# Kernel optimization log

Hardware: AMD Instinct MI355X
Metric: run time of the kernel (lower is better)

Reference implementation:

```python
import jax, jax.numpy as jnp
import numpy as np

B, N, D, H, O, K, N_USER, C = 1, 4096, 64, 4, 64, 2, 4000, 2


def setup_inputs() -> dict:
    key = jax.random.key(0)
    ks = jax.random.split(key, 7)
    h = jax.random.normal(ks[0], (B, N, D), jnp.float32)
    # dense 0/1 adjacency per heterogeneous kind, with self-loops so no row is empty
    adj = jax.random.randint(ks[1], (K, B, N, N), 0, 2).astype(jnp.float32)
    hadj = jnp.maximum(adj, jnp.eye(N, dtype=jnp.float32))
    s = 1.0 / np.sqrt(D).astype(np.float32)
    w = jax.random.normal(ks[2], (K, H, D, O), jnp.float32) * s
    a_src = jax.random.normal(ks[3], (K, H, O, 1), jnp.float32) * (1.0 / np.sqrt(O).astype(np.float32))
    a_dst = jax.random.normal(ks[4], (K, H, O, 1), jnp.float32) * (1.0 / np.sqrt(O).astype(np.float32))
    fc_w = jax.random.normal(ks[5], (C, O * K), jnp.float32) * (1.0 / np.sqrt(O * K).astype(np.float32))
    fc_b = jnp.zeros((C,), jnp.float32)
    return {"h": h, "hadj": hadj, "w": w, "a_src": a_src, "a_dst": a_dst, "fc_w": fc_w, "fc_b": fc_b}


def _gat(h, adj, w_k, a_src_k, a_dst_k):
    # h: (B,N,D); adj: (B,N,N); w_k: (H,D,O); a_*: (H,O,1)
    h_prime = jnp.einsum('bnf,hfo->bhno', h, w_k)          # (B,H,N,O)
    t = jnp.tanh(h_prime)
    attn_src = jnp.einsum('bhno,hoi->bhni', t, a_src_k)    # (B,H,N,1)
    attn_dst = jnp.einsum('bhno,hoi->bhni', t, a_dst_k)    # (B,H,N,1)
    attn = attn_src + jnp.swapaxes(attn_dst, -1, -2)       # (B,H,N,N) broadcast add
    attn = jnp.where(attn >= 0, attn, 0.2 * attn)          # LeakyReLU(0.2)
    attn = jnp.where(adj[:, None] > 0, attn, -jnp.inf)     # dense mask
    attn = jax.nn.softmax(attn, axis=-1)                   # dropout is a no-op in eval
    out = jnp.einsum('bhnm,bhmo->bhno', attn, h_prime)     # (B,H,N,O)
    return out.mean(axis=1)                                # mean over heads -> (B,N,O)


def reference(h, hadj, w, a_src, a_dst, fc_w, fc_b):
    embs = []
    for k in range(K):  # small fixed loop over heterogeneous node kinds
        x = _gat(h, hadj[k], w[k], a_src[k], a_dst[k])
        embs.append(x[:, :N_USER])
    type_aware = jnp.concatenate(embs, axis=-1)            # (B, N_USER, K*O)
    logits = type_aware @ fc_w.T + fc_b                    # (B, N_USER, C)
    return jax.nn.log_softmax(logits, axis=-1)
```

## Files before the change

### kernel.cpp

```cpp
#include <hip/hip_runtime.h>
#include <math.h>

constexpr int KK = 2;
constexpr int HH = 4;
constexpr int NN = 4096;
constexpr int DD = 64;
constexpr int OO = 64;
constexpr int NU = 4000;
constexpr int CC = 2;
constexpr int JSPLIT = 8;
constexpr int JCHUNK = NN / JSPLIT;
constexpr int NTILE = JCHUNK / 16;
constexpr float LOG2E = 1.44269504088896340736f;

typedef float vf4 __attribute__((ext_vector_type(4)));

__device__ __forceinline__ float fexp2(float x) {
#if __has_builtin(__builtin_amdgcn_exp2f)
  return __builtin_amdgcn_exp2f(x);
#else
  return exp2f(x);
#endif
}
__device__ __forceinline__ float frcp(float x) {
#if __has_builtin(__builtin_amdgcn_rcpf)
  return __builtin_amdgcn_rcpf(x);
#else
  return 1.0f / x;
#endif
}
__device__ __forceinline__ float ftanh(float x) {
  float e = fexp2(x * (2.0f * LOG2E));
  return 1.0f - 2.0f * frcp(e + 1.0f);
}

__global__ __launch_bounds__(256) void gat_phase1(
    const float* __restrict__ hsrc, const float* __restrict__ w,
    const float* __restrict__ a_src, const float* __restrict__ a_dst,
    const float* __restrict__ fc_w,
    float* __restrict__ src_s, float* __restrict__ att_d,
    float* __restrict__ att_g0, float* __restrict__ att_g1) {
  const int kh = blockIdx.y;
  const int k = kh >> 2;
  const int i0 = blockIdx.x * 64;
  const int tid = threadIdx.x;

  __shared__ float h_s[DD][68];
  __shared__ float w_s[DD][OO];

  {
    const float4* wp = (const float4*)(w + (size_t)kh * DD * OO);
    float4* ws4 = (float4*)w_s;
    for (int t = tid; t < DD * OO / 4; t += 256) ws4[t] = wp[t];
  }
  for (int t = tid; t < 1024; t += 256) {
    const int row = t >> 4;
    const int f4 = (t & 15) * 4;
    float4 v = *(const float4*)(hsrc + (size_t)(i0 + row) * DD + f4);
    h_s[f4 + 0][row] = v.x;
    h_s[f4 + 1][row] = v.y;
    h_s[f4 + 2][row] = v.z;
    h_s[f4 + 3][row] = v.w;
  }
  __syncthreads();

  const int og = tid & 15;
  const int rg = tid >> 4;
  const int o0 = og * 4;
  const int r0 = rg * 4;

  float hp[4][4];
#pragma unroll
  for (int j = 0; j < 4; ++j)
#pragma unroll
    for (int u = 0; u < 4; ++u) hp[j][u] = 0.0f;

#pragma unroll 8
  for (int f = 0; f < DD; ++f) {
    float4 hv = *(const float4*)&h_s[f][r0];
    float4 wv = *(const float4*)&w_s[f][o0];
    hp[0][0] = fmaf(hv.x, wv.x, hp[0][0]);
    hp[0][1] = fmaf(hv.x, wv.y, hp[0][1]);
    hp[0][2] = fmaf(hv.x, wv.z, hp[0][2]);
    hp[0][3] = fmaf(hv.x, wv.w, hp[0][3]);
    hp[1][0] = fmaf(hv.y, wv.x, hp[1][0]);
    hp[1][1] = fmaf(hv.y, wv.y, hp[1][1]);
    hp[1][2] = fmaf(hv.y, wv.z, hp[1][2]);
    hp[1][3] = fmaf(hv.y, wv.w, hp[1][3]);
    hp[2][0] = fmaf(hv.z, wv.x, hp[2][0]);
    hp[2][1] = fmaf(hv.z, wv.y, hp[2][1]);
    hp[2][2] = fmaf(hv.z, wv.z, hp[2][2]);
    hp[2][3] = fmaf(hv.z, wv.w, hp[2][3]);
    hp[3][0] = fmaf(hv.w, wv.x, hp[3][0]);
    hp[3][1] = fmaf(hv.w, wv.y, hp[3][1]);
    hp[3][2] = fmaf(hv.w, wv.z, hp[3][2]);
    hp[3][3] = fmaf(hv.w, wv.w, hp[3][3]);
  }

  float as[4], ad[4], f0[4], f1[4];
#pragma unroll
  for (int u = 0; u < 4; ++u) {
    as[u] = a_src[kh * OO + o0 + u];
    ad[u] = a_dst[kh * OO + o0 + u];
    f0[u] = fc_w[0 * (KK * OO) + k * OO + o0 + u];
    f1[u] = fc_w[1 * (KK * OO) + k * OO + o0 + u];
  }

#pragma unroll
  for (int j = 0; j < 4; ++j) {
    float sp = 0.0f, dp = 0.0f, g0 = 0.0f, g1 = 0.0f;
#pragma unroll
    for (int u = 0; u < 4; ++u) {
      float v = hp[j][u];
      float t = ftanh(v);
      sp = fmaf(t, as[u], sp);
      dp = fmaf(t, ad[u], dp);
      g0 = fmaf(v, f0[u], g0);
      g1 = fmaf(v, f1[u], g1);
    }
#pragma unroll
    for (int off = 1; off < 16; off <<= 1) {
      sp += __shfl_xor(sp, off, 64);
      dp += __shfl_xor(dp, off, 64);
      g0 += __shfl_xor(g0, off, 64);
      g1 += __shfl_xor(g1, off, 64);
    }
    if (og == 0) {
      const int i = i0 + r0 + j;
      src_s[kh * NN + i] = sp * LOG2E;
      att_d[kh * NN + i] = dp * LOG2E;
      att_g0[kh * NN + i] = g0;
      att_g1[kh * NN + i] = g1;
    }
  }
}

__global__ __launch_bounds__(256) void gat_phase2(
    const float* __restrict__ adj, const float* __restrict__ src_s,
    const float* __restrict__ att_d, const float* __restrict__ att_g0,
    const float* __restrict__ att_g1, float* __restrict__ P) {
  const int k = blockIdx.y >> 3;
  const int chunk = blockIdx.y & 7;
  const int r0 = blockIdx.x * 16;
  const int tid = threadIdx.x;
  const int wave = tid >> 6;
  const int lane = tid & 63;
  const int row = lane & 15;
  const int jsub = lane >> 4;
  const int i = r0 + row;
  const int j0 = chunk * JCHUNK;

  __shared__ float lds_att[12][JCHUNK];
  {
    const float* planes[3] = {att_d, att_g0, att_g1};
#pragma unroll
    for (int step = 0; step < 6; ++step) {
      const int fi = step * 256 + tid;
      const int v = fi >> 7;
      const int pos = (fi & 127) * 4;
      const int p = v >> 2, h = v & 3;
      vf4 val = *(const vf4*)(planes[p] + (size_t)(k * HH + h) * NN + j0 + pos);
      *(vf4*)&lds_att[v][pos] = val;
    }
  }

  float sreg[4];
#pragma unroll
  for (int h = 0; h < 4; ++h) sreg[h] = src_s[(k * HH + h) * NN + i];

  float l[4], a0[4], a1[4];
#pragma unroll
  for (int h = 0; h < 4; ++h) {
    l[h] = 0.0f;
    a0[h] = 0.0f;
    a1[h] = 0.0f;
  }

  __syncthreads();

  const float* arow = adj + (size_t)k * NN * NN + (size_t)i * NN + j0 + jsub * 4;
  vf4 apre0 = *(const vf4*)(arow + (wave + 0) * 16);
  vf4 apre1 = *(const vf4*)(arow + (wave + 4) * 16);

#pragma unroll
  for (int s = 0; s < 8; ++s) {
    const int t = wave + s * 4;
    const vf4 av = apre0;
    apre0 = apre1;
    if (s < 6) apre1 = *(const vf4*)(arow + (t + 8) * 16);
    const int jloc = jsub * 4 + t * 16;
#pragma unroll
    for (int h = 0; h < 4; ++h) {
      vf4 dv = *(const vf4*)&lds_att[0 * 4 + h][jloc];
      vf4 g0v = *(const vf4*)&lds_att[1 * 4 + h][jloc];
      vf4 g1v = *(const vf4*)&lds_att[2 * 4 + h][jloc];
#pragma unroll
      for (int jj = 0; jj < 4; ++jj) {
        float s2 = sreg[h] + dv[jj];
        float sl = fmaxf(s2, 0.2f * s2);
        float p = av[jj] * fexp2(sl);
        l[h] += p;
        a0[h] = fmaf(p, g0v[jj], a0[h]);
        a1[h] = fmaf(p, g1v[jj], a1[h]);
      }
    }
  }

#pragma unroll
  for (int h = 0; h < 4; ++h) {
    l[h] += __shfl_xor(l[h], 16, 64);
    l[h] += __shfl_xor(l[h], 32, 64);
    a0[h] += __shfl_xor(a0[h], 16, 64);
    a0[h] += __shfl_xor(a0[h], 32, 64);
    a1[h] += __shfl_xor(a1[h], 16, 64);
    a1[h] += __shfl_xor(a1[h], 32, 64);
  }

  __shared__ float sred[4][12][16];
  if (lane < 16) {
#pragma unroll
    for (int h = 0; h < 4; ++h) {
      sred[wave][h * 3 + 0][row] = l[h];
      sred[wave][h * 3 + 1][row] = a0[h];
      sred[wave][h * 3 + 2][row] = a1[h];
    }
  }
  __syncthreads();
  if (tid < 192) {
    const int v = tid >> 4;
    const int rr = tid & 15;
    float sum =
        sred[0][v][rr] + sred[1][v][rr] + sred[2][v][rr] + sred[3][v][rr];
    const int h = v / 3, c = v % 3;
    size_t base =
        ((((size_t)(k * JSPLIT + chunk) * HH + h) * 3 + c)) * NU + (r0 + rr);
    P[base] = sum;
  }
}

__global__ __launch_bounds__(256) void gat_phase3(
    const float* __restrict__ P, const float* __restrict__ fc_b,
    float* __restrict__ out) {
  const int i = blockIdx.x * 256 + threadIdx.x;
  if (i >= NU) return;
  float l0 = fc_b[0], l1 = fc_b[1];
#pragma unroll
  for (int k = 0; k < KK; ++k) {
#pragma unroll
    for (int q = 0; q < HH; ++q) {
      float ls = 0.0f, a0 = 0.0f, a1 = 0.0f;
#pragma unroll
      for (int ch = 0; ch < JSPLIT; ++ch) {
        size_t b = (((size_t)(k * JSPLIT + ch) * HH + q) * 3) * NU + i;
        ls += P[b];
        a0 += P[b + NU];
        a1 += P[b + 2 * (size_t)NU];
      }
      float inv = 1.0f / ls;
      l0 = fmaf(0.25f * a0, inv, l0);
      l1 = fmaf(0.25f * a1, inv, l1);
    }
  }
  float m = fmaxf(l0, l1);
  float lse = m + logf(expf(l0 - m) + expf(l1 - m));
  out[i * CC + 0] = l0 - lse;
  out[i * CC + 1] = l1 - lse;
}

extern "C" void kernel_launch(void* const* d_in, const int* in_sizes, int n_in,
                              void* d_out, int out_size, void* d_ws, size_t ws_size,
                              hipStream_t stream) {
  const float* hsrc  = (const float*)d_in[0];
  const float* hadj  = (const float*)d_in[1];
  const float* w     = (const float*)d_in[2];
  const float* a_src = (const float*)d_in[3];
  const float* a_dst = (const float*)d_in[4];
  const float* fc_w  = (const float*)d_in[5];
  const float* fc_b  = (const float*)d_in[6];
  float* out = (float*)d_out;

  char* ws = (char*)d_ws;
  float* src_s  = (float*)(ws + 0 * 131072);
  float* att_d  = (float*)(ws + 1 * 131072);
  float* att_g0 = (float*)(ws + 2 * 131072);
  float* att_g1 = (float*)(ws + 3 * 131072);
  float* P      = (float*)(ws + 4 * 131072);

  dim3 g1(NN / 64, KK * HH);
  gat_phase1<<<g1, 256, 0, stream>>>(hsrc, w, a_src, a_dst, fc_w,
                                     src_s, att_d, att_g0, att_g1);
  dim3 g2(NU / 16, KK * JSPLIT);
  gat_phase2<<<g2, 256, 0, stream>>>(hadj, src_s, att_d, att_g0, att_g1, P);
  gat_phase3<<<(NU + 255) / 256, 256, 0, stream>>>(P, fc_b, out);
}
```

Measured before the change: 222.7 us.

## Retile phase2 to 32 rows per block with packed float2 math

Phase 2 now handles 32 rows per block instead of 16. Each lane walks a row with 8-wide j stripes, so the per-row shuffle reduction drops to a single xor step and each LDS tile of attention coefficients is reused across twice as many rows. The LeakyReLU is rewritten as 0.6x + 0.4|x| and the accumulators use float2 vectors so the compiler can emit packed FMA instructions. Phase 1 is retiled to 32 rows per block for more blocks. The cost is that adjacency loads per lane are now 32-byte strided segments, which may hurt global coalescing, and phase 2 launches half as many blocks.

```diff
diff --git a/kernel.cpp b/kernel.cpp
--- a/kernel.cpp
+++ b/kernel.cpp
@@ -10,10 +10,10 @@
 constexpr int CC = 2;
 constexpr int JSPLIT = 8;
 constexpr int JCHUNK = NN / JSPLIT;
-constexpr int NTILE = JCHUNK / 16;
 constexpr float LOG2E = 1.44269504088896340736f;
 
 typedef float vf4 __attribute__((ext_vector_type(4)));
+typedef float vf2 __attribute__((ext_vector_type(2)));
 
 __device__ __forceinline__ float fexp2(float x) {
 #if __has_builtin(__builtin_amdgcn_exp2f)
@@ -42,21 +42,23 @@
     float* __restrict__ att_g0, float* __restrict__ att_g1) {
   const int kh = blockIdx.y;
   const int k = kh >> 2;
-  const int i0 = blockIdx.x * 64;
+  const int i0 = blockIdx.x * 32;
   const int tid = threadIdx.x;
 
-  __shared__ float h_s[DD][68];
+  __shared__ float h_s[DD][36];
   __shared__ float w_s[DD][OO];
 
   {
-    const float4* wp = (const float4*)(w + (size_t)kh * DD * OO);
-    float4* ws4 = (float4*)w_s;
+    const vf4* wp = (const vf4*)(w + (size_t)kh * DD * OO);
+    vf4* ws4 = (vf4*)w_s;
+#pragma unroll
     for (int t = tid; t < DD * OO / 4; t += 256) ws4[t] = wp[t];
   }
-  for (int t = tid; t < 1024; t += 256) {
+#pragma unroll
+  for (int t = tid; t < 512; t += 256) {
     const int row = t >> 4;
     const int f4 = (t & 15) * 4;
-    float4 v = *(const float4*)(hsrc + (size_t)(i0 + row) * DD + f4);
+    vf4 v = *(const vf4*)(hsrc + (size_t)(i0 + row) * DD + f4);
     h_s[f4 + 0][row] = v.x;
     h_s[f4 + 1][row] = v.y;
     h_s[f4 + 2][row] = v.z;
@@ -67,18 +69,18 @@
   const int og = tid & 15;
   const int rg = tid >> 4;
   const int o0 = og * 4;
-  const int r0 = rg * 4;
-
-  float hp[4][4];
-#pragma unroll
-  for (int j = 0; j < 4; ++j)
+  const int r0 = rg * 2;
+
+  float hp[2][4];
+#pragma unroll
+  for (int j = 0; j < 2; ++j)
 #pragma unroll
     for (int u = 0; u < 4; ++u) hp[j][u] = 0.0f;
 
 #pragma unroll 8
   for (int f = 0; f < DD; ++f) {
-    float4 hv = *(const float4*)&h_s[f][r0];
-    float4 wv = *(const float4*)&w_s[f][o0];
+    vf2 hv = *(const vf2*)&h_s[f][r0];
+    vf4 wv = *(const vf4*)&w_s[f][o0];
     hp[0][0] = fmaf(hv.x, wv.x, hp[0][0]);
     hp[0][1] = fmaf(hv.x, wv.y, hp[0][1]);
     hp[0][2] = fmaf(hv.x, wv.z, hp[0][2]);
@@ -87,14 +89,6 @@
     hp[1][1] = fmaf(hv.y, wv.y, hp[1][1]);
     hp[1][2] = fmaf(hv.y, wv.z, hp[1][2]);
     hp[1][3] = fmaf(hv.y, wv.w, hp[1][3]);
-    hp[2][0] = fmaf(hv.z, wv.x, hp[2][0]);
-    hp[2][1] = fmaf(hv.z, wv.y, hp[2][1]);
-    hp[2][2] = fmaf(hv.z, wv.z, hp[2][2]);
-    hp[2][3] = fmaf(hv.z, wv.w, hp[2][3]);
-    hp[3][0] = fmaf(hv.w, wv.x, hp[3][0]);
-    hp[3][1] = fmaf(hv.w, wv.y, hp[3][1]);
-    hp[3][2] = fmaf(hv.w, wv.z, hp[3][2]);
-    hp[3][3] = fmaf(hv.w, wv.w, hp[3][3]);
   }
 
   float as[4], ad[4], f0[4], f1[4];
@@ -107,7 +101,7 @@
   }
 
 #pragma unroll
-  for (int j = 0; j < 4; ++j) {
+  for (int j = 0; j < 2; ++j) {
     float sp = 0.0f, dp = 0.0f, g0 = 0.0f, g1 = 0.0f;
 #pragma unroll
     for (int u = 0; u < 4; ++u) {
@@ -141,12 +135,12 @@
     const float* __restrict__ att_g1, float* __restrict__ P) {
   const int k = blockIdx.y >> 3;
   const int chunk = blockIdx.y & 7;
-  const int r0 = blockIdx.x * 16;
+  const int r0 = blockIdx.x * 32;
   const int tid = threadIdx.x;
   const int wave = tid >> 6;
   const int lane = tid & 63;
-  const int row = lane & 15;
-  const int jsub = lane >> 4;
+  const int row = lane & 31;
+  const int jsub = lane >> 5;
   const int i = r0 + row;
   const int j0 = chunk * JCHUNK;
 
@@ -164,60 +158,77 @@
     }
   }
 
-  float sreg[4];
-#pragma unroll
-  for (int h = 0; h < 4; ++h) sreg[h] = src_s[(k * HH + h) * NN + i];
-
-  float l[4], a0[4], a1[4];
+  vf2 sreg2[4];
 #pragma unroll
   for (int h = 0; h < 4; ++h) {
-    l[h] = 0.0f;
-    a0[h] = 0.0f;
-    a1[h] = 0.0f;
+    float s = src_s[(k * HH + h) * NN + i];
+    sreg2[h].x = s;
+    sreg2[h].y = s;
+  }
+
+  vf2 l2[4], a02[4], a12[4];
+#pragma unroll
+  for (int h = 0; h < 4; ++h) {
+    l2[h] = (vf2)(0.0f);
+    a02[h] = (vf2)(0.0f);
+    a12[h] = (vf2)(0.0f);
   }
 
   __syncthreads();
 
-  const float* arow = adj + (size_t)k * NN * NN + (size_t)i * NN + j0 + jsub * 4;
-  vf4 apre0 = *(const vf4*)(arow + (wave + 0) * 16);
-  vf4 apre1 = *(const vf4*)(arow + (wave + 4) * 16);
-
-#pragma unroll
-  for (int s = 0; s < 8; ++s) {
+  const float* arow =
+      adj + (size_t)k * NN * NN + (size_t)i * NN + j0 + jsub * 4;
+  vf4 apre0 = *(const vf4*)(arow + (wave + 0) * 8);
+  vf4 apre1 = *(const vf4*)(arow + (wave + 4) * 8);
+
+#pragma unroll 4
+  for (int s = 0; s < 16; ++s) {
     const int t = wave + s * 4;
     const vf4 av = apre0;
     apre0 = apre1;
-    if (s < 6) apre1 = *(const vf4*)(arow + (t + 8) * 16);
-    const int jloc = jsub * 4 + t * 16;
+    if (s < 14) apre1 = *(const vf4*)(arow + (wave + (s + 2) * 4) * 8);
+    const int jloc = t * 8 + jsub * 4;
 #pragma unroll
     for (int h = 0; h < 4; ++h) {
       vf4 dv = *(const vf4*)&lds_att[0 * 4 + h][jloc];
       vf4 g0v = *(const vf4*)&lds_att[1 * 4 + h][jloc];
       vf4 g1v = *(const vf4*)&lds_att[2 * 4 + h][jloc];
 #pragma unroll
-      for (int jj = 0; jj < 4; ++jj) {
-        float s2 = sreg[h] + dv[jj];
-        float sl = fmaxf(s2, 0.2f * s2);
-        float p = av[jj] * fexp2(sl);
-        l[h] += p;
-        a0[h] = fmaf(p, g0v[jj], a0[h]);
-        a1[h] = fmaf(p, g1v[jj], a1[h]);
+      for (int pp = 0; pp < 2; ++pp) {
+        vf2 dpair = {dv[2 * pp], dv[2 * pp + 1]};
+        vf2 apair = {av[2 * pp], av[2 * pp + 1]};
+        vf2 g0p = {g0v[2 * pp], g0v[2 * pp + 1]};
+        vf2 g1p = {g1v[2 * pp], g1v[2 * pp + 1]};
+        vf2 s2 = sreg2[h] + dpair;
+        vf2 t6 = s2 * 0.6f;
+        vf2 e;
+        e.x = fexp2(fmaf(0.4f, __builtin_fabsf(s2.x), t6.x));
+        e.y = fexp2(fmaf(0.4f, __builtin_fabsf(s2.y), t6.y));
+        vf2 p2 = apair * e;
+        l2[h] += p2;
+        a02[h] = __builtin_elementwise_fma(p2, g0p, a02[h]);
+        a12[h] = __builtin_elementwise_fma(p2, g1p, a12[h]);
       }
     }
   }
 
+  float l[4], a0[4], a1[4];
 #pragma unroll
   for (int h = 0; h < 4; ++h) {
-    l[h] += __shfl_xor(l[h], 16, 64);
-    l[h] += __shfl_xor(l[h], 32, 64);
-    a0[h] += __shfl_xor(a0[h], 16, 64);
-    a0[h] += __shfl_xor(a0[h], 32, 64);
-    a1[h] += __shfl_xor(a1[h], 16, 64);
-    a1[h] += __shfl_xor(a1[h], 32, 64);
-  }
-
-  __shared__ float sred[4][12][16];
-  if (lane < 16) {
+    vf2 x0 = l2[h], x1 = a02[h], x2 = a12[h];
+    x0.x += __shfl_xor(x0.x, 32, 64);
+    x0.y += __shfl_xor(x0.y, 32, 64);
+    x1.x += __shfl_xor(x1.x, 32, 64);
+    x1.y += __shfl_xor(x1.y, 32, 64);
+    x2.x += __shfl_xor(x2.x, 32, 64);
+    x2.y += __shfl_xor(x2.y, 32, 64);
+    l[h] = x0.x + x0.y;
+    a0[h] = x1.x + x1.y;
+    a1[h] = x2.x + x2.y;
+  }
+
+  __shared__ float sred[4][12][32];
+  if (lane < 32) {
 #pragma unroll
     for (int h = 0; h < 4; ++h) {
       sred[wave][h * 3 + 0][row] = l[h];
@@ -226,9 +237,10 @@
     }
   }
   __syncthreads();
-  if (tid < 192) {
-    const int v = tid >> 4;
-    const int rr = tid & 15;
+#pragma unroll
+  for (int idx = tid; idx < 384; idx += 256) {
+    const int v = idx >> 5;
+    const int rr = idx & 31;
     float sum =
         sred[0][v][rr] + sred[1][v][rr] + sred[2][v][rr] + sred[3][v][rr];
     const int h = v / 3, c = v % 3;
@@ -286,10 +298,10 @@
   float* att_g1 = (float*)(ws + 3 * 131072);
   float* P      = (float*)(ws + 4 * 131072);
 
-  dim3 g1(NN / 64, KK * HH);
+  dim3 g1(NN / 32, KK * HH);
   gat_phase1<<<g1, 256, 0, stream>>>(hsrc, w, a_src, a_dst, fc_w,
                                      src_s, att_d, att_g0, att_g1);
-  dim3 g2(NU / 16, KK * JSPLIT);
+  dim3 g2(NU / 32, KK * JSPLIT);
   gat_phase2<<<g2, 256, 0, stream>>>(hadj, src_s, att_d, att_g0, att_g1, P);
   gat_phase3<<<(NU + 255) / 256, 256, 0, stream>>>(P, fc_b, out);
 }
```

New measurement: 236.5 us. +6.2%, slower.
